# Kernel tuning notes

Measured on AMD Instinct MI355X. Metric: run time of the kernel, lower is better.

Reference implementation:

```python
import jax, jax.numpy as jnp
import numpy as np

B, L, D = 2, 2048, 1024
H = 16
HD = D // H  # 64


def _orthogonal_projection(key, d, m):
    g = jax.random.normal(key, (d, m), dtype=jnp.float32)
    q, r = jnp.linalg.qr(g)
    s = jnp.sign(jnp.diagonal(r))
    s = jnp.where(s == 0, 1.0, s)
    q = q * s[None, :]
    # preserve_variance=True
    return q * np.sqrt(d / m)


def setup_inputs() -> dict:
    key = jax.random.key(0)
    ks = jax.random.split(key, 8)
    x = jax.random.normal(ks[0], (B, L, D), dtype=jnp.float32)
    p = jax.random.normal(ks[1], (B, L, D), dtype=jnp.float32)
    s = 1.0 / np.sqrt(D)
    W_qkv = jax.random.uniform(ks[2], (3 * D, D), dtype=jnp.float32, minval=-s, maxval=s)
    b_qkv = jax.random.uniform(ks[3], (3 * D,), dtype=jnp.float32, minval=-s, maxval=s)
    W_out = jax.random.uniform(ks[4], (D, D), dtype=jnp.float32, minval=-s, maxval=s)
    b_out = jax.random.uniform(ks[5], (D,), dtype=jnp.float32, minval=-s, maxval=s)
    proj = _orthogonal_projection(ks[6], D, D // 2)
    return {"x": x, "p": p, "W_qkv": W_qkv, "b_qkv": b_qkv,
            "W_out": W_out, "b_out": b_out, "proj": proj}


def reference(x, p, W_qkv, b_qkv, W_out, b_out, proj):
    # QKV projection: (B,L,D) -> (B,L,3,H,HD)
    qkv = (jnp.einsum('bld,ed->ble', x, W_qkv) + b_qkv).reshape(B, L, 3, H, HD)
    q, k, v = qkv[:, :, 0], qkv[:, :, 1], qkv[:, :, 2]

    # Collaborative rotary phases from conditioning tokens: (B,L,H,HD/2)
    phases = (p @ proj).reshape(B, L, H, HD // 2)  # phase_scale = 1.0
    cos, sin = jnp.cos(phases), jnp.sin(phases)

    half = HD // 2
    # non-interleaved rotary: split head_dim into two halves
    def rot(t):
        t1, t2 = t[..., :half], t[..., half:]
        return jnp.concatenate([t1 * cos - t2 * sin, t1 * sin + t2 * cos], axis=-1)

    q, k = rot(q), rot(k)

    scale = HD ** -0.5
    scores = jnp.einsum('bqhd,bkhd->bhqk', q, k) * scale
    attn = jax.nn.softmax(scores, axis=-1)
    out = jnp.einsum('bhqk,bkhd->bqhd', attn, v).reshape(B, L, D)
    return jnp.einsum('bld,ed->ble', out, W_out) + b_out
```

## Files before the change

kernel.cpp:

```cpp
#include <hip/hip_runtime.h>
#include <hip/hip_bf16.h>
#include <math.h>

namespace {
constexpr int Bb = 2;
constexpr int Ll = 2048;
constexpr int Dd = 1024;
constexpr int Hh = 16;
constexpr int NT = Bb * Ll;
constexpr int D3 = 3 * Dd;
constexpr int PH = Dd / 2;
constexpr int LDK = 72;
}

typedef __attribute__((ext_vector_type(8))) short bf16x8;
typedef __attribute__((ext_vector_type(4))) short bf16x4;
typedef __attribute__((ext_vector_type(4))) float f32x4;

#if defined(__has_builtin)
#if __has_builtin(__builtin_amdgcn_mfma_f32_16x16x16bf16_1k)
#define HAVE_MFMA16 1
#endif
#endif

__device__ inline unsigned pack2bf(float a, float b) {
  __hip_bfloat162 t = __float22bfloat162_rn(float2{a, b});
  union { __hip_bfloat162 h; unsigned u; } cv; cv.h = t;
  return cv.u;
}

__device__ inline bf16x4 u2bf4(uint2 u) {
  union { uint2 u; bf16x4 v; } c; c.u = u; return c.v;
}

__device__ inline f32x4 pv_mfma(bf16x4 va, bf16x4 vb, f32x4 c) {
#ifdef HAVE_MFMA16
  return __builtin_amdgcn_mfma_f32_16x16x16bf16_1k(va, vb, c, 0, 0, 0);
#else
  const bf16x8 a8 = {va[0], va[1], va[2], va[3], 0, 0, 0, 0};
  const bf16x8 b8 = {vb[0], vb[1], vb[2], vb[3], 0, 0, 0, 0};
  return __builtin_amdgcn_mfma_f32_16x16x32_bf16(a8, b8, c, 0, 0, 0);
#endif
}

__device__ inline void async_cp16(const void* gsrc, void* ldst) {
  __builtin_amdgcn_global_load_lds(
      (const __attribute__((address_space(1))) unsigned int*)gsrc,
      (__attribute__((address_space(3))) unsigned int*)ldst, 16, 0, 0);
}

__global__ __launch_bounds__(256) void prep_kernel(
    const float4* __restrict__ p, uint2* __restrict__ p_hi4, uint2* __restrict__ p_lo4,
    const float* __restrict__ proj, short* __restrict__ th, short* __restrict__ tl,
    const float4* __restrict__ x, const float4* __restrict__ wq, const float4* __restrict__ wo,
    uint2* __restrict__ xd, uint2* __restrict__ wqd, uint2* __restrict__ wod)
{
  __shared__ float Ls[64][65];
  const int bid = blockIdx.x;
  const int tid = threadIdx.x;

  if (bid < 4096) {
    const int i = bid * 256 + tid;
    const float4 f = p[i];
    float hf[4], lf[4];
    const float ff[4] = {f.x, f.y, f.z, f.w};
#pragma unroll
    for (int j = 0; j < 4; ++j) {
      const __hip_bfloat16 h = __float2bfloat16(ff[j]);
      hf[j] = __bfloat162float(h);
      lf[j] = ff[j] - hf[j];
    }
    p_hi4[i] = make_uint2(pack2bf(hf[0], hf[1]), pack2bf(hf[2], hf[3]));
    p_lo4[i] = make_uint2(pack2bf(lf[0], lf[1]), pack2bf(lf[2], lf[3]));
  } else if (bid < 4224) {
    const int bx = bid - 4096;
    const int d0 = (bx & 15) * 64, m0 = (bx >> 4) * 64;
    const int r = tid >> 4, c4 = (tid & 15) * 4;
#pragma unroll
    for (int it = 0; it < 4; ++it) {
      const int row = it * 16 + r;
      const float4 v = *(const float4*)&proj[(size_t)(d0 + row) * PH + m0 + c4];
      Ls[row][c4] = v.x; Ls[row][c4+1] = v.y; Ls[row][c4+2] = v.z; Ls[row][c4+3] = v.w;
    }
    __syncthreads();
#pragma unroll
    for (int it = 0; it < 4; ++it) {
      const int row = it * 16 + r;
      float hf[4], lf[4];
#pragma unroll
      for (int j = 0; j < 4; ++j) {
        const float v = Ls[c4 + j][row];
        const __hip_bfloat16 h = __float2bfloat16(v);
        hf[j] = __bfloat162float(h);
        lf[j] = v - hf[j];
      }
      *(uint2*)&th[(size_t)(m0 + row) * Dd + d0 + c4] = make_uint2(pack2bf(hf[0], hf[1]), pack2bf(hf[2], hf[3]));
      *(uint2*)&tl[(size_t)(m0 + row) * Dd + d0 + c4] = make_uint2(pack2bf(lf[0], lf[1]), pack2bf(lf[2], lf[3]));
    }
  } else {
    int i = (bid - 4224) * 256 + tid;
    const float4* s; uint2* d;
    if (i < 1048576) { s = x; d = xd; }
    else if (i < 1048576 + 786432) { i -= 1048576; s = wq; d = wqd; }
    else { i -= 1048576 + 786432; s = wo; d = wod; }
    const float4 f = s[i];
    d[i] = make_uint2(pack2bf(f.x, f.y), pack2bf(f.z, f.w));
  }
}

__global__ __launch_bounds__(256) void gemm_nn_split(
    const short* __restrict__ Ah_g, const short* __restrict__ Al_g,
    const short* __restrict__ Wh_g, const short* __restrict__ Wl_g,
    float* __restrict__ C)
{
  __shared__ __align__(16) short Ah[128 * 32], Al[128 * 32], Wh[64 * 32], Wl[64 * 32];
  const int tid = threadIdx.x;
  const int w = tid >> 6, lane = tid & 63;
  const int l15 = lane & 15, quad = lane >> 4;
  const int n0 = blockIdx.y * 128, m0 = blockIdx.x * 64;

  const int row = tid >> 2, cc = tid & 3;
  const int ksw = (cc ^ (row & 3)) * 8;
  const short* gAh = Ah_g + (size_t)(n0 + row) * Dd + ksw;
  const short* gAl = Al_g + (size_t)(n0 + row) * Dd + ksw;
  const short* gWh = Wh_g + (size_t)(m0 + row) * Dd + ksw;
  const short* gWl = Wl_g + (size_t)(m0 + row) * Dd + ksw;
  short* lAh  = Ah + tid * 8;
  short* lAh2 = Ah + 2048 + tid * 8;
  short* lAl  = Al + tid * 8;
  short* lAl2 = Al + 2048 + tid * 8;
  short* lWh  = Wh + tid * 8;
  short* lWl  = Wl + tid * 8;

  f32x4 acc[2][4];
#pragma unroll
  for (int i = 0; i < 2; ++i)
#pragma unroll
    for (int j = 0; j < 4; ++j) acc[i][j] = f32x4{0.f, 0.f, 0.f, 0.f};

  const int swq = (quad ^ (l15 & 3)) * 8;

  for (int k0 = 0; k0 < Dd; k0 += 32) {
    __syncthreads();
    async_cp16(gAh + k0, lAh);
    async_cp16(gAh + 64 * Dd + k0, lAh2);
    async_cp16(gAl + k0, lAl);
    async_cp16(gAl + 64 * Dd + k0, lAl2);
    async_cp16(gWh + k0, lWh);
    async_cp16(gWl + k0, lWl);
    __syncthreads();

    bf16x8 ah[2], al[2], wh[4], wl[4];
#pragma unroll
    for (int i = 0; i < 2; ++i) {
      ah[i] = *(const bf16x8*)&Ah[(w * 32 + i * 16 + l15) * 32 + swq];
      al[i] = *(const bf16x8*)&Al[(w * 32 + i * 16 + l15) * 32 + swq];
    }
#pragma unroll
    for (int j = 0; j < 4; ++j) {
      wh[j] = *(const bf16x8*)&Wh[(j * 16 + l15) * 32 + swq];
      wl[j] = *(const bf16x8*)&Wl[(j * 16 + l15) * 32 + swq];
    }
#pragma unroll
    for (int i = 0; i < 2; ++i)
#pragma unroll
      for (int j = 0; j < 4; ++j) {
        acc[i][j] = __builtin_amdgcn_mfma_f32_16x16x32_bf16(ah[i], wh[j], acc[i][j], 0, 0, 0);
        acc[i][j] = __builtin_amdgcn_mfma_f32_16x16x32_bf16(ah[i], wl[j], acc[i][j], 0, 0, 0);
        acc[i][j] = __builtin_amdgcn_mfma_f32_16x16x32_bf16(al[i], wh[j], acc[i][j], 0, 0, 0);
      }
  }

#pragma unroll
  for (int i = 0; i < 2; ++i)
#pragma unroll
    for (int r = 0; r < 4; ++r) {
      float* crow = C + (size_t)(n0 + w * 32 + i * 16 + quad * 4 + r) * PH + m0 + l15;
#pragma unroll
      for (int j = 0; j < 4; ++j) crow[j * 16] = acc[i][j][r];
    }
}

__global__ __launch_bounds__(256) void gemm_qkv_fused(
    const __hip_bfloat16* __restrict__ A, const __hip_bfloat16* __restrict__ W,
    const float* __restrict__ bias, const float* __restrict__ phases,
    __hip_bfloat16* __restrict__ q_bf, __hip_bfloat16* __restrict__ k_bf,
    __hip_bfloat16* __restrict__ vt_g)
{
  __shared__ __align__(16) short As[128 * 32];
  __shared__ __align__(16) short Ws[128 * 32];
  const int tid = threadIdx.x;
  const int w = tid >> 6, lane = tid & 63;
  const int l15 = lane & 15, quad = lane >> 4;
  const int wn = w >> 1, wm = w & 1;
  const int n0 = blockIdx.y * 128, m0 = blockIdx.x * 128;

  const int row = tid >> 2, cc = tid & 3;
  const int ksw = (cc ^ (row & 3)) * 8;
  const short* gA  = (const short*)A + (size_t)(n0 + row) * Dd + ksw;
  const short* gW  = (const short*)W + (size_t)(m0 + row) * Dd + ksw;
  short* lA  = As + tid * 8;
  short* lA2 = As + 2048 + tid * 8;
  short* lW  = Ws + tid * 8;
  short* lW2 = Ws + 2048 + tid * 8;

  f32x4 acc[4][4];
#pragma unroll
  for (int i = 0; i < 4; ++i)
#pragma unroll
    for (int j = 0; j < 4; ++j) acc[i][j] = f32x4{0.f, 0.f, 0.f, 0.f};

  const int swq = (quad ^ (l15 & 3)) * 8;

  for (int k0 = 0; k0 < Dd; k0 += 32) {
    __syncthreads();
    async_cp16(gA + k0, lA);
    async_cp16(gA + 64 * Dd + k0, lA2);
    async_cp16(gW + k0, lW);
    async_cp16(gW + 64 * Dd + k0, lW2);
    __syncthreads();

    bf16x8 af[4], bf[4];
#pragma unroll
    for (int i = 0; i < 4; ++i)
      af[i] = *(const bf16x8*)&As[(wn * 64 + i * 16 + l15) * 32 + swq];
#pragma unroll
    for (int j = 0; j < 4; ++j)
      bf[j] = *(const bf16x8*)&Ws[(wm * 64 + j * 16 + l15) * 32 + swq];
#pragma unroll
    for (int i = 0; i < 4; ++i)
#pragma unroll
      for (int j = 0; j < 4; ++j)
        acc[i][j] = __builtin_amdgcn_mfma_f32_16x16x32_bf16(af[i], bf[j], acc[i][j], 0, 0, 0);
  }

  float bv[4];
#pragma unroll
  for (int j = 0; j < 4; ++j) bv[j] = bias[m0 + wm * 64 + j * 16 + l15];

  const int region = m0 >> 10;
  const int mloc = (m0 & 1023) + wm * 64;
  const int h = mloc >> 6;

  if (region < 2) {
    __hip_bfloat16* dst = region == 0 ? q_bf : k_bf;
    const float SC = region == 0 ? 0.18033688011112042f : 1.0f;
#pragma unroll
    for (int i = 0; i < 4; ++i)
#pragma unroll
      for (int r = 0; r < 4; ++r) {
        const int n = n0 + wn * 64 + i * 16 + quad * 4 + r;
        const float* phrow = phases + (size_t)n * PH + h * 32;
        __hip_bfloat16* drow = dst + (size_t)n * Dd + h * 64;
#pragma unroll
        for (int pz = 0; pz < 2; ++pz) {
          const float ph = phrow[pz * 16 + l15];
          float sn, cs;
          __sincosf(ph, &sn, &cs);
          const float a1 = acc[i][pz][r] + bv[pz];
          const float a2 = acc[i][pz + 2][r] + bv[pz + 2];
          drow[pz * 16 + l15]      = __float2bfloat16((a1 * cs - a2 * sn) * SC);
          drow[pz * 16 + 32 + l15] = __float2bfloat16((a1 * sn + a2 * cs) * SC);
        }
      }
  } else {
    const int bh = (n0 >> 11) * 16 + h;
    const int tokb = (n0 & 2047) + wn * 64;
#pragma unroll
    for (int i = 0; i < 4; ++i)
#pragma unroll
      for (int j = 0; j < 4; ++j) {
        const uint2 o = make_uint2(
            pack2bf(acc[i][j][0] + bv[j], acc[i][j][1] + bv[j]),
            pack2bf(acc[i][j][2] + bv[j], acc[i][j][3] + bv[j]));
        const int d = j * 16 + l15;
        *(uint2*)&vt_g[(size_t)(bh * 64 + d) * Ll + tokb + i * 16 + quad * 4] = o;
      }
  }
}

__global__ __launch_bounds__(256) void gemm_bt_bf16(
    const __hip_bfloat16* __restrict__ A, const __hip_bfloat16* __restrict__ W,
    const float* __restrict__ bias, float* __restrict__ C, int K, int M)
{
  __shared__ __align__(16) short As[128 * 32];
  __shared__ __align__(16) short Ws[128 * 32];
  const int tid = threadIdx.x;
  const int w = tid >> 6, lane = tid & 63;
  const int l15 = lane & 15, quad = lane >> 4;
  const int wn = w >> 1, wm = w & 1;
  const int n0 = blockIdx.y * 128, m0 = blockIdx.x * 128;

  const int row = tid >> 2, cc = tid & 3;
  const int ksw = (cc ^ (row & 3)) * 8;
  const short* gA  = (const short*)A + (size_t)(n0 + row) * K + ksw;
  const short* gW  = (const short*)W + (size_t)(m0 + row) * K + ksw;
  short* lA  = As + tid * 8;
  short* lA2 = As + 2048 + tid * 8;
  short* lW  = Ws + tid * 8;
  short* lW2 = Ws + 2048 + tid * 8;

  f32x4 acc[4][4];
#pragma unroll
  for (int i = 0; i < 4; ++i)
#pragma unroll
    for (int j = 0; j < 4; ++j) acc[i][j] = f32x4{0.f, 0.f, 0.f, 0.f};

  const int swq = (quad ^ (l15 & 3)) * 8;

  for (int k0 = 0; k0 < K; k0 += 32) {
    __syncthreads();
    async_cp16(gA + k0, lA);
    async_cp16(gA + 64 * K + k0, lA2);
    async_cp16(gW + k0, lW);
    async_cp16(gW + 64 * K + k0, lW2);
    __syncthreads();

    bf16x8 af[4], bf[4];
#pragma unroll
    for (int i = 0; i < 4; ++i)
      af[i] = *(const bf16x8*)&As[(wn * 64 + i * 16 + l15) * 32 + swq];
#pragma unroll
    for (int j = 0; j < 4; ++j)
      bf[j] = *(const bf16x8*)&Ws[(wm * 64 + j * 16 + l15) * 32 + swq];
#pragma unroll
    for (int i = 0; i < 4; ++i)
#pragma unroll
      for (int j = 0; j < 4; ++j)
        acc[i][j] = __builtin_amdgcn_mfma_f32_16x16x32_bf16(af[i], bf[j], acc[i][j], 0, 0, 0);
  }

  float bv[4];
#pragma unroll
  for (int j = 0; j < 4; ++j) bv[j] = bias[m0 + wm * 64 + j * 16 + l15];
#pragma unroll
  for (int i = 0; i < 4; ++i)
#pragma unroll
    for (int r = 0; r < 4; ++r) {
      float* crow = C + (size_t)(n0 + wn * 64 + i * 16 + quad * 4 + r) * M + m0 + wm * 64 + l15;
#pragma unroll
      for (int j = 0; j < 4; ++j) crow[j * 16] = acc[i][j][r] + bv[j];
    }
}

__global__ __launch_bounds__(256) void attn_mfma(
    const __hip_bfloat16* __restrict__ q_bf,
    const __hip_bfloat16* __restrict__ k_bf,
    const __hip_bfloat16* __restrict__ vt_g,
    __hip_bfloat16* __restrict__ aout)
{
  __shared__ __align__(16) short Ks[2][64 * LDK];
  __shared__ __align__(16) short Vt[2][64 * LDK];

  const int tid = threadIdx.x;
  const int w = tid >> 6;
  const int lane = tid & 63;
  const int l15 = lane & 15;
  const int quad = lane >> 4;

  const int q0 = blockIdx.x * 128;
  const int bh = blockIdx.y;
  const int b = bh >> 4, h = bh & 15;

  bf16x8 qfrag[2][2];
#pragma unroll
  for (int qg = 0; qg < 2; ++qg)
#pragma unroll
    for (int kh = 0; kh < 2; ++kh) {
      const size_t qrow = (size_t)(b * Ll + q0 + w * 32 + qg * 16 + l15);
      qfrag[qg][kh] = *(const bf16x8*)(q_bf + qrow * Dd + h * 64 + kh * 32 + quad * 8);
    }

  f32x4 acc[4][2];
#pragma unroll
  for (int dt = 0; dt < 4; ++dt)
#pragma unroll
    for (int qg = 0; qg < 2; ++qg) acc[dt][qg] = f32x4{0.f, 0.f, 0.f, 0.f};
  f32x4 lden[2] = {f32x4{0.f,0.f,0.f,0.f}, f32x4{0.f,0.f,0.f,0.f}};
  const short one_bf = (short)0x3F80;
  const bf16x4 ones = {one_bf, one_bf, one_bf, one_bf};

  const int srow = tid >> 2, sseg = tid & 3;
  const __hip_bfloat16* kbase = k_bf + (size_t)(b * Ll + srow) * Dd + h * 64 + sseg * 16;
  const __hip_bfloat16* vbase = vt_g + ((size_t)(bh * 64 + srow)) * Ll + sseg * 16;
  const int soff = srow * LDK + sseg * 16;

  uint4 pk0, pk1, pv0, pv1;
  {
    const uint4* kg = (const uint4*)kbase;
    pk0 = kg[0]; pk1 = kg[1];
    const uint4* vg = (const uint4*)vbase;
    pv0 = vg[0]; pv1 = vg[1];
    *(uint4*)&Ks[0][soff]     = pk0;
    *(uint4*)&Ks[0][soff + 8] = pk1;
    *(uint4*)&Vt[0][soff]     = pv0;
    *(uint4*)&Vt[0][soff + 8] = pv1;
  }
  {
    const uint4* kg = (const uint4*)(kbase + (size_t)64 * Dd);
    pk0 = kg[0]; pk1 = kg[1];
    const uint4* vg = (const uint4*)(vbase + 64);
    pv0 = vg[0]; pv1 = vg[1];
  }

  for (int kt = 0; kt < Ll / 64; ++kt) {
    const int cur = kt & 1, nxt = cur ^ 1;
    __syncthreads();
    *(uint4*)&Ks[nxt][soff]     = pk0;
    *(uint4*)&Ks[nxt][soff + 8] = pk1;
    *(uint4*)&Vt[nxt][soff]     = pv0;
    *(uint4*)&Vt[nxt][soff + 8] = pv1;
    {
      const int ktn = (kt + 2) & 31;
      const uint4* kg = (const uint4*)(kbase + (size_t)ktn * 64 * Dd);
      pk0 = kg[0]; pk1 = kg[1];
      const uint4* vg = (const uint4*)(vbase + ktn * 64);
      pv0 = vg[0]; pv1 = vg[1];
    }

    f32x4 s[4][2];
#pragma unroll
    for (int n = 0; n < 4; ++n)
#pragma unroll
      for (int qg = 0; qg < 2; ++qg) s[n][qg] = f32x4{0.f, 0.f, 0.f, 0.f};
#pragma unroll
    for (int n = 0; n < 4; ++n)
#pragma unroll
      for (int kh = 0; kh < 2; ++kh) {
        const bf16x8 af = *(const bf16x8*)&Ks[cur][(n * 16 + l15) * LDK + kh * 32 + quad * 8];
        s[n][0] = __builtin_amdgcn_mfma_f32_16x16x32_bf16(af, qfrag[0][kh], s[n][0], 0, 0, 0);
        s[n][1] = __builtin_amdgcn_mfma_f32_16x16x32_bf16(af, qfrag[1][kh], s[n][1], 0, 0, 0);
      }

    uint2 bq[4][2];
#pragma unroll
    for (int qg = 0; qg < 2; ++qg)
#pragma unroll
      for (int n = 0; n < 4; ++n) {
        union { float f; unsigned u; } p0, p1, p2, p3;
        p0.f = __builtin_amdgcn_exp2f(s[n][qg][0]);
        p1.f = __builtin_amdgcn_exp2f(s[n][qg][1]);
        p2.f = __builtin_amdgcn_exp2f(s[n][qg][2]);
        p3.f = __builtin_amdgcn_exp2f(s[n][qg][3]);
        bq[n][qg] = make_uint2(__builtin_amdgcn_perm(p1.u, p0.u, 0x07060302u),
                               __builtin_amdgcn_perm(p3.u, p2.u, 0x07060302u));
      }

#pragma unroll
    for (int n = 0; n < 4; ++n) {
      const bf16x4 pb0 = u2bf4(bq[n][0]);
      const bf16x4 pb1 = u2bf4(bq[n][1]);
      lden[0] = pv_mfma(ones, pb0, lden[0]);
      lden[1] = pv_mfma(ones, pb1, lden[1]);
#pragma unroll
      for (int dt = 0; dt < 4; ++dt) {
        const bf16x4 va = *(const bf16x4*)&Vt[cur][(dt * 16 + l15) * LDK + n * 16 + quad * 4];
        acc[dt][0] = pv_mfma(va, pb0, acc[dt][0]);
        acc[dt][1] = pv_mfma(va, pb1, acc[dt][1]);
      }
    }
  }

#pragma unroll
  for (int qg = 0; qg < 2; ++qg) {
    const float linv = 1.f / lden[qg][0];
    const size_t q = (size_t)(b * Ll + q0 + w * 32 + qg * 16 + l15);
#pragma unroll
    for (int dt = 0; dt < 4; ++dt) {
      const uint2 o = make_uint2(
          pack2bf(acc[dt][qg][0] * linv, acc[dt][qg][1] * linv),
          pack2bf(acc[dt][qg][2] * linv, acc[dt][qg][3] * linv));
      *(uint2*)&aout[q * Dd + h * 64 + dt * 16 + quad * 4] = o;
    }
  }
}

extern "C" void kernel_launch(void* const* d_in, const int* in_sizes, int n_in,
                              void* d_out, int out_size, void* d_ws, size_t ws_size,
                              hipStream_t stream) {
  const float* x     = (const float*)d_in[0];
  const float* p     = (const float*)d_in[1];
  const float* W_qkv = (const float*)d_in[2];
  const float* b_qkv = (const float*)d_in[3];
  const float* W_out = (const float*)d_in[4];
  const float* b_out = (const float*)d_in[5];
  const float* proj  = (const float*)d_in[6];
  float* out = (float*)d_out;

  char* wsb = (char*)d_ws;
  float*          phases   = (float*)(wsb);
  short*          p_hi     = (short*)(wsb + (8u << 20));
  __hip_bfloat16* aout_bf  = (__hip_bfloat16*)(wsb + (8u << 20));
  short*          p_lo     = (short*)(wsb + (16u << 20));
  __hip_bfloat16* vt_g     = (__hip_bfloat16*)(wsb + (16u << 20));
  short*          projt_hi = (short*)(wsb + (24u << 20));
  short*          projt_lo = (short*)(wsb + (25u << 20));
  __hip_bfloat16* q_bf     = (__hip_bfloat16*)(wsb + (26u << 20));
  __hip_bfloat16* k_bf     = (__hip_bfloat16*)(wsb + (34u << 20));
  __hip_bfloat16* x_bf     = (__hip_bfloat16*)(wsb + (42u << 20));
  __hip_bfloat16* wqkv_bf  = (__hip_bfloat16*)(wsb + (50u << 20));
  __hip_bfloat16* wout_bf  = (__hip_bfloat16*)(wsb + (56u << 20));

  prep_kernel<<<12416, 256, 0, stream>>>(
      (const float4*)p, (uint2*)p_hi, (uint2*)p_lo,
      proj, projt_hi, projt_lo,
      (const float4*)x, (const float4*)W_qkv, (const float4*)W_out,
      (uint2*)x_bf, (uint2*)wqkv_bf, (uint2*)wout_bf);
  gemm_nn_split<<<dim3(PH / 64, NT / 128), 256, 0, stream>>>(p_hi, p_lo, projt_hi, projt_lo, phases);
  gemm_qkv_fused<<<dim3(D3 / 128, NT / 128), 256, 0, stream>>>(x_bf, wqkv_bf, b_qkv, phases,
                                                               q_bf, k_bf, vt_g);
  attn_mfma<<<dim3(Ll / 128, Bb * Hh), 256, 0, stream>>>(q_bf, k_bf, vt_g, aout_bf);
  gemm_bt_bf16<<<dim3(Dd / 128, NT / 128), 256, 0, stream>>>(aout_bf, wout_bf, b_out, out, Dd, Dd);
}
```

Baseline: 270.7 us.

## Split attention over key halves with combine kernel; shrink output GEMM tile

Attention now runs as split-K over the key dimension: a third grid dimension of 2 gives each block half the keys. Each block writes a normalized partial output plus its softmax denominator, and a new combine kernel merges the halves with denominator-weighted averaging. The attention K/V shared buffers drop from double to single buffering, with an extra barrier per tile. The output projection GEMM uses 128x64 tiles, doubling its block count for better CU occupancy, at the cost of an extra kernel launch, extra global traffic for the partials and an extra bf16 rounding step.

```diff
diff --git a/kernel.cpp b/kernel.cpp
--- a/kernel.cpp
+++ b/kernel.cpp
@@ -31,6 +31,12 @@
 
 __device__ inline bf16x4 u2bf4(uint2 u) {
   union { uint2 u; bf16x4 v; } c; c.u = u; return c.v;
+}
+
+__device__ inline float bfhalf(unsigned u, int hi) {
+  union { unsigned u; float f; } c;
+  c.u = hi ? (u & 0xffff0000u) : (u << 16);
+  return c.f;
 }
 
 __device__ inline f32x4 pv_mfma(bf16x4 va, bf16x4 vb, f32x4 c) {
@@ -279,30 +285,28 @@
   }
 }
 
-__global__ __launch_bounds__(256) void gemm_bt_bf16(
+__global__ __launch_bounds__(256) void gemm_bt_64(
     const __hip_bfloat16* __restrict__ A, const __hip_bfloat16* __restrict__ W,
     const float* __restrict__ bias, float* __restrict__ C, int K, int M)
 {
   __shared__ __align__(16) short As[128 * 32];
-  __shared__ __align__(16) short Ws[128 * 32];
+  __shared__ __align__(16) short Ws[64 * 32];
   const int tid = threadIdx.x;
   const int w = tid >> 6, lane = tid & 63;
   const int l15 = lane & 15, quad = lane >> 4;
-  const int wn = w >> 1, wm = w & 1;
-  const int n0 = blockIdx.y * 128, m0 = blockIdx.x * 128;
+  const int n0 = blockIdx.y * 128, m0 = blockIdx.x * 64;
 
   const int row = tid >> 2, cc = tid & 3;
   const int ksw = (cc ^ (row & 3)) * 8;
-  const short* gA  = (const short*)A + (size_t)(n0 + row) * K + ksw;
-  const short* gW  = (const short*)W + (size_t)(m0 + row) * K + ksw;
+  const short* gA = (const short*)A + (size_t)(n0 + row) * K + ksw;
+  const short* gW = (const short*)W + (size_t)(m0 + row) * K + ksw;
   short* lA  = As + tid * 8;
   short* lA2 = As + 2048 + tid * 8;
   short* lW  = Ws + tid * 8;
-  short* lW2 = Ws + 2048 + tid * 8;
-
-  f32x4 acc[4][4];
-#pragma unroll
-  for (int i = 0; i < 4; ++i)
+
+  f32x4 acc[2][4];
+#pragma unroll
+  for (int i = 0; i < 2; ++i)
 #pragma unroll
     for (int j = 0; j < 4; ++j) acc[i][j] = f32x4{0.f, 0.f, 0.f, 0.f};
 
@@ -313,18 +317,17 @@
     async_cp16(gA + k0, lA);
     async_cp16(gA + 64 * K + k0, lA2);
     async_cp16(gW + k0, lW);
-    async_cp16(gW + 64 * K + k0, lW2);
-    __syncthreads();
-
-    bf16x8 af[4], bf[4];
-#pragma unroll
-    for (int i = 0; i < 4; ++i)
-      af[i] = *(const bf16x8*)&As[(wn * 64 + i * 16 + l15) * 32 + swq];
+    __syncthreads();
+
+    bf16x8 af[2], bf[4];
+#pragma unroll
+    for (int i = 0; i < 2; ++i)
+      af[i] = *(const bf16x8*)&As[(w * 32 + i * 16 + l15) * 32 + swq];
 #pragma unroll
     for (int j = 0; j < 4; ++j)
-      bf[j] = *(const bf16x8*)&Ws[(wm * 64 + j * 16 + l15) * 32 + swq];
-#pragma unroll
-    for (int i = 0; i < 4; ++i)
+      bf[j] = *(const bf16x8*)&Ws[(j * 16 + l15) * 32 + swq];
+#pragma unroll
+    for (int i = 0; i < 2; ++i)
 #pragma unroll
       for (int j = 0; j < 4; ++j)
         acc[i][j] = __builtin_amdgcn_mfma_f32_16x16x32_bf16(af[i], bf[j], acc[i][j], 0, 0, 0);
@@ -332,12 +335,12 @@
 
   float bv[4];
 #pragma unroll
-  for (int j = 0; j < 4; ++j) bv[j] = bias[m0 + wm * 64 + j * 16 + l15];
-#pragma unroll
-  for (int i = 0; i < 4; ++i)
+  for (int j = 0; j < 4; ++j) bv[j] = bias[m0 + j * 16 + l15];
+#pragma unroll
+  for (int i = 0; i < 2; ++i)
 #pragma unroll
     for (int r = 0; r < 4; ++r) {
-      float* crow = C + (size_t)(n0 + wn * 64 + i * 16 + quad * 4 + r) * M + m0 + wm * 64 + l15;
+      float* crow = C + (size_t)(n0 + w * 32 + i * 16 + quad * 4 + r) * M + m0 + l15;
 #pragma unroll
       for (int j = 0; j < 4; ++j) crow[j * 16] = acc[i][j][r] + bv[j];
     }
@@ -347,10 +350,11 @@
     const __hip_bfloat16* __restrict__ q_bf,
     const __hip_bfloat16* __restrict__ k_bf,
     const __hip_bfloat16* __restrict__ vt_g,
-    __hip_bfloat16* __restrict__ aout)
+    __hip_bfloat16* __restrict__ o_part,
+    float* __restrict__ lden_g)
 {
-  __shared__ __align__(16) short Ks[2][64 * LDK];
-  __shared__ __align__(16) short Vt[2][64 * LDK];
+  __shared__ __align__(16) short Ks[64 * LDK];
+  __shared__ __align__(16) short Vt[64 * LDK];
 
   const int tid = threadIdx.x;
   const int w = tid >> 6;
@@ -360,7 +364,9 @@
 
   const int q0 = blockIdx.x * 128;
   const int bh = blockIdx.y;
+  const int kz = blockIdx.z;
   const int b = bh >> 4, h = bh & 15;
+  const int kt0 = kz * 16;
 
   bf16x8 qfrag[2][2];
 #pragma unroll
@@ -383,35 +389,25 @@
   const int srow = tid >> 2, sseg = tid & 3;
   const __hip_bfloat16* kbase = k_bf + (size_t)(b * Ll + srow) * Dd + h * 64 + sseg * 16;
   const __hip_bfloat16* vbase = vt_g + ((size_t)(bh * 64 + srow)) * Ll + sseg * 16;
-  const int soff = srow * LDK + sseg * 16;
 
   uint4 pk0, pk1, pv0, pv1;
   {
-    const uint4* kg = (const uint4*)kbase;
+    const uint4* kg = (const uint4*)(kbase + (size_t)kt0 * 64 * Dd);
     pk0 = kg[0]; pk1 = kg[1];
-    const uint4* vg = (const uint4*)vbase;
+    const uint4* vg = (const uint4*)(vbase + kt0 * 64);
     pv0 = vg[0]; pv1 = vg[1];
-    *(uint4*)&Ks[0][soff]     = pk0;
-    *(uint4*)&Ks[0][soff + 8] = pk1;
-    *(uint4*)&Vt[0][soff]     = pv0;
-    *(uint4*)&Vt[0][soff + 8] = pv1;
-  }
-  {
-    const uint4* kg = (const uint4*)(kbase + (size_t)64 * Dd);
-    pk0 = kg[0]; pk1 = kg[1];
-    const uint4* vg = (const uint4*)(vbase + 64);
-    pv0 = vg[0]; pv1 = vg[1];
-  }
-
-  for (int kt = 0; kt < Ll / 64; ++kt) {
-    const int cur = kt & 1, nxt = cur ^ 1;
-    __syncthreads();
-    *(uint4*)&Ks[nxt][soff]     = pk0;
-    *(uint4*)&Ks[nxt][soff + 8] = pk1;
-    *(uint4*)&Vt[nxt][soff]     = pv0;
-    *(uint4*)&Vt[nxt][soff + 8] = pv1;
+  }
+
+  for (int kt = 0; kt < 16; ++kt) {
+    __syncthreads();
+    *(uint4*)&Ks[srow * LDK + sseg * 16]     = pk0;
+    *(uint4*)&Ks[srow * LDK + sseg * 16 + 8] = pk1;
+    *(uint4*)&Vt[srow * LDK + sseg * 16]     = pv0;
+    *(uint4*)&Vt[srow * LDK + sseg * 16 + 8] = pv1;
+    __syncthreads();
+
     {
-      const int ktn = (kt + 2) & 31;
+      const int ktn = kt0 + ((kt + 1) & 15);
       const uint4* kg = (const uint4*)(kbase + (size_t)ktn * 64 * Dd);
       pk0 = kg[0]; pk1 = kg[1];
       const uint4* vg = (const uint4*)(vbase + ktn * 64);
@@ -427,7 +423,7 @@
     for (int n = 0; n < 4; ++n)
 #pragma unroll
       for (int kh = 0; kh < 2; ++kh) {
-        const bf16x8 af = *(const bf16x8*)&Ks[cur][(n * 16 + l15) * LDK + kh * 32 + quad * 8];
+        const bf16x8 af = *(const bf16x8*)&Ks[(n * 16 + l15) * LDK + kh * 32 + quad * 8];
         s[n][0] = __builtin_amdgcn_mfma_f32_16x16x32_bf16(af, qfrag[0][kh], s[n][0], 0, 0, 0);
         s[n][1] = __builtin_amdgcn_mfma_f32_16x16x32_bf16(af, qfrag[1][kh], s[n][1], 0, 0, 0);
       }
@@ -454,7 +450,7 @@
       lden[1] = pv_mfma(ones, pb1, lden[1]);
 #pragma unroll
       for (int dt = 0; dt < 4; ++dt) {
-        const bf16x4 va = *(const bf16x4*)&Vt[cur][(dt * 16 + l15) * LDK + n * 16 + quad * 4];
+        const bf16x4 va = *(const bf16x4*)&Vt[(dt * 16 + l15) * LDK + n * 16 + quad * 4];
         acc[dt][0] = pv_mfma(va, pb0, acc[dt][0]);
         acc[dt][1] = pv_mfma(va, pb1, acc[dt][1]);
       }
@@ -463,16 +459,41 @@
 
 #pragma unroll
   for (int qg = 0; qg < 2; ++qg) {
-    const float linv = 1.f / lden[qg][0];
-    const size_t q = (size_t)(b * Ll + q0 + w * 32 + qg * 16 + l15);
+    const float lv = lden[qg][0];
+    const float linv = 1.f / lv;
+    const int ql = q0 + w * 32 + qg * 16 + l15;
+    if (quad == 0)
+      lden_g[((size_t)(kz * Bb + b) * Hh + h) * Ll + ql] = lv;
+    __hip_bfloat16* dst = o_part + ((size_t)kz * NT + b * Ll + ql) * Dd + h * 64;
 #pragma unroll
     for (int dt = 0; dt < 4; ++dt) {
       const uint2 o = make_uint2(
           pack2bf(acc[dt][qg][0] * linv, acc[dt][qg][1] * linv),
           pack2bf(acc[dt][qg][2] * linv, acc[dt][qg][3] * linv));
-      *(uint2*)&aout[q * Dd + h * 64 + dt * 16 + quad * 4] = o;
-    }
-  }
+      *(uint2*)&dst[dt * 16 + quad * 4] = o;
+    }
+  }
+}
+
+__global__ __launch_bounds__(256) void attn_combine(
+    const __hip_bfloat16* __restrict__ o_part, const float* __restrict__ lden_g,
+    __hip_bfloat16* __restrict__ aout)
+{
+  const int i = blockIdx.x * 256 + threadIdx.x;
+  const int n = i >> 8, d4 = i & 255;
+  const int b = n >> 11, l = n & 2047;
+  const int h = d4 >> 4;
+  const float l0 = lden_g[((size_t)b * Hh + h) * Ll + l];
+  const float l1 = lden_g[((size_t)(Bb + b) * Hh + h) * Ll + l];
+  const float inv = 1.f / (l0 + l1);
+  const float w0 = l0 * inv, w1 = l1 * inv;
+  const uint2 a0 = ((const uint2*)o_part)[i];
+  const uint2 a1 = ((const uint2*)o_part)[(NT * (size_t)Dd / 4) + i];
+  const float r0 = w0 * bfhalf(a0.x, 0) + w1 * bfhalf(a1.x, 0);
+  const float r1 = w0 * bfhalf(a0.x, 1) + w1 * bfhalf(a1.x, 1);
+  const float r2 = w0 * bfhalf(a0.y, 0) + w1 * bfhalf(a1.y, 0);
+  const float r3 = w0 * bfhalf(a0.y, 1) + w1 * bfhalf(a1.y, 1);
+  ((uint2*)aout)[i] = make_uint2(pack2bf(r0, r1), pack2bf(r2, r3));
 }
 
 extern "C" void kernel_launch(void* const* d_in, const int* in_sizes, int n_in,
@@ -498,8 +519,10 @@
   __hip_bfloat16* q_bf     = (__hip_bfloat16*)(wsb + (26u << 20));
   __hip_bfloat16* k_bf     = (__hip_bfloat16*)(wsb + (34u << 20));
   __hip_bfloat16* x_bf     = (__hip_bfloat16*)(wsb + (42u << 20));
+  __hip_bfloat16* o_part   = (__hip_bfloat16*)(wsb + (42u << 20));
   __hip_bfloat16* wqkv_bf  = (__hip_bfloat16*)(wsb + (50u << 20));
-  __hip_bfloat16* wout_bf  = (__hip_bfloat16*)(wsb + (56u << 20));
+  __hip_bfloat16* wout_bf  = (__hip_bfloat16*)(wsb + (58u << 20));
+  float*          lden_g   = (float*)(wsb + (60u << 20));
 
   prep_kernel<<<12416, 256, 0, stream>>>(
       (const float4*)p, (uint2*)p_hi, (uint2*)p_lo,
@@ -509,6 +532,7 @@
   gemm_nn_split<<<dim3(PH / 64, NT / 128), 256, 0, stream>>>(p_hi, p_lo, projt_hi, projt_lo, phases);
   gemm_qkv_fused<<<dim3(D3 / 128, NT / 128), 256, 0, stream>>>(x_bf, wqkv_bf, b_qkv, phases,
                                                                q_bf, k_bf, vt_g);
-  attn_mfma<<<dim3(Ll / 128, Bb * Hh), 256, 0, stream>>>(q_bf, k_bf, vt_g, aout_bf);
-  gemm_bt_bf16<<<dim3(Dd / 128, NT / 128), 256, 0, stream>>>(aout_bf, wout_bf, b_out, out, Dd, Dd);
-}
+  attn_mfma<<<dim3(Ll / 128, Bb * Hh, 2), 256, 0, stream>>>(q_bf, k_bf, vt_g, o_part, lden_g);
+  attn_combine<<<4096, 256, 0, stream>>>(o_part, lden_g, aout_bf);
+  gemm_bt_64<<<dim3(Dd / 64, NT / 128), 256, 0, stream>>>(aout_bf, wout_bf, b_out, out, Dd, Dd);
+}
```

New measurement: 262.7 us. 1.03x faster.
